# Kernel tuning notes

Hardware: AMD Instinct MI355X
Metric: run time of the kernel (lower is better)

## Reference

```python
import jax, jax.numpy as jnp
import numpy as np

# Real spherical-harmonics constants (degree 4, 16 basis functions),
# matching the torch-ngp / nr3d_lib CUDA shencoder coefficients.
C0 = 0.28209479177387814
C1 = 0.4886025119029199
C2 = (1.0925484305920792, -1.0925484305920792, 0.31539156525252005,
      -1.0925484305920792, 0.5462742152960396)
C3 = (-0.5900435899266435, 2.890611442640554, -0.4570457994644658,
      0.3731763325901154, -0.4570457994644658, 1.445305721320277,
      -0.5900435899266435)


def sh_encode_deg4(p):
    # p: [B, 3] -> [B, 16]
    x, y, z = p[:, 0], p[:, 1], p[:, 2]
    xx, yy, zz = x * x, y * y, z * z
    xy, yz, xz = x * y, y * z, x * z
    ones = jnp.ones_like(x)
    cols = [
        C0 * ones,
        -C1 * y,
        C1 * z,
        -C1 * x,
        C2[0] * xy,
        C2[1] * yz,
        C2[2] * (2.0 * zz - xx - yy),
        C2[3] * xz,
        C2[4] * (xx - yy),
        C3[0] * y * (3.0 * xx - yy),
        C3[1] * xy * z,
        C3[2] * y * (4.0 * zz - xx - yy),
        C3[3] * z * (2.0 * zz - 3.0 * xx - 3.0 * yy),
        C3[4] * x * (4.0 * zz - xx - yy),
        C3[5] * z * (xx - yy),
        C3[6] * x * (xx - 3.0 * yy),
    ]
    return jnp.stack(cols, axis=-1)


def setup_inputs() -> dict:
    key = jax.random.key(0)
    B = 4194304
    inputs = jax.random.normal(key, (B, 3), dtype=jnp.float32)
    return {"inputs": inputs, "size": 1}


def reference(inputs, size):
    prefix = inputs.shape[:-1]
    p = (inputs / size).reshape(-1, 3)
    out = sh_encode_deg4(p)  # [B, 16]
    return out.reshape(*prefix, 16)
```

## Files before the change

kernel.cpp:

```cpp
#include <hip/hip_runtime.h>


#define ROUND_POINTS 256
#define ROUNDS       4
#define LDS_STRIDE   20

__device__ __forceinline__ void sh16(float x, float y, float z,
                                     float4& o0, float4& o1,
                                     float4& o2, float4& o3) {
    const float xx = x * x, yy = y * y, zz = z * z;
    const float xy = x * y, yz = y * z, xz = x * z;

    o0.x = 0.28209479177387814f;
    o0.y = -0.4886025119029199f * y;
    o0.z =  0.4886025119029199f * z;
    o0.w = -0.4886025119029199f * x;

    o1.x =  1.0925484305920792f  * xy;
    o1.y = -1.0925484305920792f  * yz;
    o1.z =  0.31539156525252005f * (2.0f * zz - xx - yy);
    o1.w = -1.0925484305920792f  * xz;

    o2.x =  0.5462742152960396f  * (xx - yy);
    o2.y = -0.5900435899266435f  * y * (3.0f * xx - yy);
    o2.z =  2.890611442640554f   * xy * z;
    o2.w = -0.4570457994644658f  * y * (4.0f * zz - xx - yy);

    o3.x =  0.3731763325901154f  * z * (2.0f * zz - 3.0f * xx - 3.0f * yy);
    o3.y = -0.4570457994644658f  * x * (4.0f * zz - xx - yy);
    o3.z =  1.445305721320277f   * z * (xx - yy);
    o3.w = -0.5900435899266435f  * x * (xx - 3.0f * yy);
}

__global__ __launch_bounds__(256)
void SHEncoder_53077205844617_kernel(const float* __restrict__ in,
                                     float* __restrict__ out,
                                     const int* __restrict__ size_ptr,
                                     int B) {
    __shared__ float sh[ROUND_POINTS * LDS_STRIDE];

    const int t     = threadIdx.x;
    const int tile0 = blockIdx.x * (ROUND_POINTS * ROUNDS);
    const float inv = 1.0f / (float)(*size_ptr);
    float4* __restrict__ out4 = (float4*)out;

    for (int j = 0; j < ROUNDS; ++j) {
        const int p = tile0 + j * ROUND_POINTS + t;
        if (p < B) {
            const float x = in[3 * p + 0] * inv;
            const float y = in[3 * p + 1] * inv;
            const float z = in[3 * p + 2] * inv;
            float4 o0, o1, o2, o3;
            sh16(x, y, z, o0, o1, o2, o3);
            float4* s = (float4*)&sh[t * LDS_STRIDE];
            s[0] = o0; s[1] = o1; s[2] = o2; s[3] = o3;
        }
        __syncthreads();

        const int qbase = (tile0 + j * ROUND_POINTS) * 4;
        const int qlim  = B * 4;
#pragma unroll
        for (int r = 0; r < 4; ++r) {
            const int ql = t + r * ROUND_POINTS;
            const int pl = ql >> 2;
            const int c  = ql & 3;
            const float4 v = *(const float4*)&sh[pl * LDS_STRIDE + 4 * c];
            const int qg = qbase + ql;
            if (qg < qlim) out4[qg] = v;
        }
        __syncthreads();
    }
}

extern "C" void kernel_launch(void* const* d_in, const int* in_sizes, int n_in,
                              void* d_out, int out_size, void* d_ws, size_t ws_size,
                              hipStream_t stream) {
    const float* in       = (const float*)d_in[0];
    const int*   size_ptr = (const int*)d_in[1];
    float*       out      = (float*)d_out;

    const int B    = in_sizes[0] / 3;
    const int tile = ROUND_POINTS * ROUNDS;
    const int blocks = (B + tile - 1) / tile;

    SHEncoder_53077205844617_kernel<<<blocks, 256, 0, stream>>>(in, out, size_ptr, B);
}
```

Baseline: 67.73 us.

## Replace LDS transpose with per-lane quarter computation in a grid-stride loop

Drops the shared-memory staging and both block barriers. Each group of four lanes now loads the same point, and each lane computes one float4 quarter of the 16 outputs, so a wavefront writes 64 contiguous float4s directly. The launch becomes a grid-stride loop capped at 2048 blocks. In exchange, input loads and shared products are repeated four times per point, and the switch on lane index causes divergence inside the wavefront.

```diff
diff --git a/kernel.cpp b/kernel.cpp
--- a/kernel.cpp
+++ b/kernel.cpp
@@ -1,74 +1,63 @@
 #include <hip/hip_runtime.h>
 
-
-#define ROUND_POINTS 256
-#define ROUNDS       4
-#define LDS_STRIDE   20
-
-__device__ __forceinline__ void sh16(float x, float y, float z,
-                                     float4& o0, float4& o1,
-                                     float4& o2, float4& o3) {
-    const float xx = x * x, yy = y * y, zz = z * z;
-    const float xy = x * y, yz = y * z, xz = x * z;
-
-    o0.x = 0.28209479177387814f;
-    o0.y = -0.4886025119029199f * y;
-    o0.z =  0.4886025119029199f * z;
-    o0.w = -0.4886025119029199f * x;
-
-    o1.x =  1.0925484305920792f  * xy;
-    o1.y = -1.0925484305920792f  * yz;
-    o1.z =  0.31539156525252005f * (2.0f * zz - xx - yy);
-    o1.w = -1.0925484305920792f  * xz;
-
-    o2.x =  0.5462742152960396f  * (xx - yy);
-    o2.y = -0.5900435899266435f  * y * (3.0f * xx - yy);
-    o2.z =  2.890611442640554f   * xy * z;
-    o2.w = -0.4570457994644658f  * y * (4.0f * zz - xx - yy);
-
-    o3.x =  0.3731763325901154f  * z * (2.0f * zz - 3.0f * xx - 3.0f * yy);
-    o3.y = -0.4570457994644658f  * x * (4.0f * zz - xx - yy);
-    o3.z =  1.445305721320277f   * z * (xx - yy);
-    o3.w = -0.5900435899266435f  * x * (xx - 3.0f * yy);
-}
 
 __global__ __launch_bounds__(256)
 void SHEncoder_53077205844617_kernel(const float* __restrict__ in,
                                      float* __restrict__ out,
                                      const int* __restrict__ size_ptr,
                                      int B) {
-    __shared__ float sh[ROUND_POINTS * LDS_STRIDE];
+    const int lane = threadIdx.x & 63;
+    const int wid  = blockIdx.x * (blockDim.x >> 6) + (threadIdx.x >> 6);
+    const int nw   = gridDim.x * (blockDim.x >> 6);
 
-    const int t     = threadIdx.x;
-    const int tile0 = blockIdx.x * (ROUND_POINTS * ROUNDS);
     const float inv = 1.0f / (float)(*size_ptr);
     float4* __restrict__ out4 = (float4*)out;
 
-    for (int j = 0; j < ROUNDS; ++j) {
-        const int p = tile0 + j * ROUND_POINTS + t;
+    const int sub = lane >> 2;
+    const int c   = lane & 3;
+    const int ntiles = (B + 15) >> 4;
+
+    for (int tile = wid; tile < ntiles; tile += nw) {
+        const int p = tile * 16 + sub;
+        float x = 0.f, y = 0.f, z = 0.f;
         if (p < B) {
-            const float x = in[3 * p + 0] * inv;
-            const float y = in[3 * p + 1] * inv;
-            const float z = in[3 * p + 2] * inv;
-            float4 o0, o1, o2, o3;
-            sh16(x, y, z, o0, o1, o2, o3);
-            float4* s = (float4*)&sh[t * LDS_STRIDE];
-            s[0] = o0; s[1] = o1; s[2] = o2; s[3] = o3;
+            x = in[3 * p + 0] * inv;
+            y = in[3 * p + 1] * inv;
+            z = in[3 * p + 2] * inv;
         }
-        __syncthreads();
+        const float xx = x * x, yy = y * y, zz = z * z;
+        const float xy = x * y, yz = y * z, xz = x * z;
 
-        const int qbase = (tile0 + j * ROUND_POINTS) * 4;
-        const int qlim  = B * 4;
-#pragma unroll
-        for (int r = 0; r < 4; ++r) {
-            const int ql = t + r * ROUND_POINTS;
-            const int pl = ql >> 2;
-            const int c  = ql & 3;
-            const float4 v = *(const float4*)&sh[pl * LDS_STRIDE + 4 * c];
-            const int qg = qbase + ql;
-            if (qg < qlim) out4[qg] = v;
+        float4 o;
+        switch (c) {
+        case 0:
+            o.x = 0.28209479177387814f;
+            o.y = -0.4886025119029199f * y;
+            o.z =  0.4886025119029199f * z;
+            o.w = -0.4886025119029199f * x;
+            break;
+        case 1:
+            o.x =  1.0925484305920792f  * xy;
+            o.y = -1.0925484305920792f  * yz;
+            o.z =  0.31539156525252005f * (2.0f * zz - xx - yy);
+            o.w = -1.0925484305920792f  * xz;
+            break;
+        case 2:
+            o.x =  0.5462742152960396f  * (xx - yy);
+            o.y = -0.5900435899266435f  * y * (3.0f * xx - yy);
+            o.z =  2.890611442640554f   * xy * z;
+            o.w = -0.4570457994644658f  * y * (4.0f * zz - xx - yy);
+            break;
+        default:
+            o.x =  0.3731763325901154f  * z * (2.0f * zz - 3.0f * xx - 3.0f * yy);
+            o.y = -0.4570457994644658f  * x * (4.0f * zz - xx - yy);
+            o.z =  1.445305721320277f   * z * (xx - yy);
+            o.w = -0.5900435899266435f  * x * (xx - 3.0f * yy);
+            break;
         }
-        __syncthreads();
+
+        const int qg = tile * 64 + lane;
+        if (qg < 4 * B) out4[qg] = o;
     }
 }
 
@@ -79,9 +68,14 @@
     const int*   size_ptr = (const int*)d_in[1];
     float*       out      = (float*)d_out;
 
-    const int B    = in_sizes[0] / 3;
-    const int tile = ROUND_POINTS * ROUNDS;
-    const int blocks = (B + tile - 1) / tile;
+    const int B = in_sizes[0] / 3;
 
-    SHEncoder_53077205844617_kernel<<<blocks, 256, 0, stream>>>(in, out, size_ptr, B);
+    const int threads = 256;
+    const int ntiles  = (B + 15) >> 4;
+    const int waves_needed = ntiles;
+    int blocks = (waves_needed + 3) / 4;
+    if (blocks > 2048) blocks = 2048;
+    if (blocks < 1) blocks = 1;
+
+    SHEncoder_53077205844617_kernel<<<blocks, threads, 0, stream>>>(in, out, size_ptr, B);
 }
```

New measurement: 69.35 us. +2.4%, slower.
